# Performance work log

Hardware: AMD Instinct MI355X
Metric: run time of the kernel (lower is better)

## Reference

```python
import jax, jax.numpy as jnp
import numpy as np

B, S, D, H, F = 2, 2048, 1024, 16, 4096
DH = D // H
EPS = 1e-6


def layer_norm(x, g, b):
    mu = jnp.mean(x, axis=-1, keepdims=True)
    var = jnp.mean(jnp.square(x - mu), axis=-1, keepdims=True)
    return (x - mu) * jax.lax.rsqrt(var + EPS) * g + b


def setup_inputs() -> dict:
    key = jax.random.key(0)
    ks = jax.random.split(key, 12)
    s_in = 1.0 / np.sqrt(D)
    s_ff = 1.0 / np.sqrt(F)
    return {
        "x_enc": jax.random.normal(ks[0], (B, S, D), jnp.float32),
        "x_pos": jax.random.normal(ks[1], (B, S, D), jnp.float32),
        "wq": jax.random.normal(ks[2], (D, D), jnp.float32) * s_in,
        "bq": jnp.zeros((D,), jnp.float32),
        "wk": jax.random.normal(ks[3], (D, D), jnp.float32) * s_in,
        "bk": jnp.zeros((D,), jnp.float32),
        "wv": jax.random.normal(ks[4], (D, D), jnp.float32) * s_in,
        "bv": jnp.zeros((D,), jnp.float32),
        "wc": jax.random.normal(ks[5], (D, D), jnp.float32) * s_in,
        "bc": jnp.zeros((D,), jnp.float32),
        "w1": jax.random.normal(ks[6], (D, F), jnp.float32) * s_in,
        "b1": jnp.zeros((F,), jnp.float32),
        "w2": jax.random.normal(ks[7], (F, D), jnp.float32) * s_ff,
        "b2": jnp.zeros((D,), jnp.float32),
        "g1": jnp.ones((D,), jnp.float32),
        "be1": jnp.zeros((D,), jnp.float32),
        "g2": jnp.ones((D,), jnp.float32),
        "be2": jnp.zeros((D,), jnp.float32),
    }


def reference(x_enc, x_pos, wq, bq, wk, bk, wv, bv, wc, bc, w1, b1, w2, b2, g1, be1, g2, be2):
    x = x_enc + x_pos  # [B,S,D]

    def split_heads(t):  # [B,S,D] -> [B,H,S,DH]
        return t.reshape(B, S, H, DH).transpose(0, 2, 1, 3)

    q = split_heads(x @ wq + bq)
    k = split_heads(x @ wk + bk)
    v = split_heads(x @ wv + bv)

    scale = jax.lax.rsqrt(jnp.asarray(DH, jnp.float32))
    logits = jnp.einsum("bhqd,bhkd->bhqk", q, k) * scale  # [B,H,S,S]
    weights = jax.nn.softmax(logits, axis=-1)
    attn = jnp.einsum("bhqk,bhkd->bhqd", weights, v)  # [B,H,S,DH]
    attn = attn.transpose(0, 2, 1, 3).reshape(B, S, D)
    attn = attn @ wc + bc

    # residual: x + LN(attn_out)   (dropout inactive in eval)
    a = x + layer_norm(attn, g1, be1)
    ffn = jnp.maximum(a @ w1 + b1, 0.0) @ w2 + b2
    out = a + layer_norm(ffn, g2, be2)
    return out
```

## Files before the change

### kernel.cpp

```cpp
#include <hip/hip_runtime.h>
#include <math.h>

#define B_ 2
#define S_ 2048
#define D_ 1024
#define H_ 16
#define F_ 4096

typedef __bf16 bf16_t;
typedef __bf16 bf16x8 __attribute__((ext_vector_type(8)));
typedef __bf16 bf16x4 __attribute__((ext_vector_type(4)));
typedef float f32x4 __attribute__((ext_vector_type(4)));
typedef float f32x16 __attribute__((ext_vector_type(16)));
typedef _Float16 f16x4 __attribute__((ext_vector_type(4)));
typedef _Float16 f16x8 __attribute__((ext_vector_type(8)));
typedef __fp16 h16x2 __attribute__((ext_vector_type(2)));

__device__ __forceinline__ bf16_t f2b(float f) { return (bf16_t)f; }

__device__ __forceinline__ void gld_lds16(const void* g, void* l) {
  __builtin_amdgcn_global_load_lds(
      (const __attribute__((address_space(1))) unsigned int*)g,
      (__attribute__((address_space(3))) unsigned int*)l, 16, 0, 0);
}

__device__ __forceinline__ void transpose_tile(const float* __restrict__ in,
                                               bf16_t* __restrict__ out,
                                               int K, int N, int bx, int by) {
  __shared__ float tile[64][65];
  int k0 = by * 64, n0 = bx * 64;
  int tid = threadIdx.x;
  int col4 = tid & 15;
  int row = tid >> 4;
#pragma unroll
  for (int rr = 0; rr < 4; ++rr) {
    int r = rr * 16 + row;
    float4 v = *reinterpret_cast<const float4*>(in + (size_t)(k0 + r) * N + n0 + col4 * 4);
    tile[r][col4 * 4 + 0] = v.x;
    tile[r][col4 * 4 + 1] = v.y;
    tile[r][col4 * 4 + 2] = v.z;
    tile[r][col4 * 4 + 3] = v.w;
  }
  __syncthreads();
#pragma unroll
  for (int rr = 0; rr < 4; ++rr) {
    int n = rr * 16 + row;
    bf16x4 o;
    o[0] = f2b(tile[col4 * 4 + 0][n]);
    o[1] = f2b(tile[col4 * 4 + 1][n]);
    o[2] = f2b(tile[col4 * 4 + 2][n]);
    o[3] = f2b(tile[col4 * 4 + 3][n]);
    *reinterpret_cast<bf16x4*>(out + (size_t)(n0 + n) * K + k0 + col4 * 4) = o;
  }
}

__global__ __launch_bounds__(256) void prep_kernel(
    const float* __restrict__ xe, const float* __restrict__ xp,
    bf16_t* __restrict__ XB,
    const float* __restrict__ wq, const float* __restrict__ wk,
    const float* __restrict__ wv, const float* __restrict__ wc,
    const float* __restrict__ w1, const float* __restrict__ w2,
    const float* __restrict__ bq, const float* __restrict__ bk,
    const float* __restrict__ bv,
    bf16_t* __restrict__ Wqkvt, bf16_t* __restrict__ wctb,
    bf16_t* __restrict__ w1tb, bf16_t* __restrict__ w2tb,
    float* __restrict__ bqkv) {
  int bid = blockIdx.x;
  if (bid < 4096) {
    int i = bid * 256 + threadIdx.x;
    float4 av = reinterpret_cast<const float4*>(xe)[i];
    float4 bv4 = reinterpret_cast<const float4*>(xp)[i];
    bf16x4 o;
    o[0] = f2b(av.x + bv4.x); o[1] = f2b(av.y + bv4.y);
    o[2] = f2b(av.z + bv4.z); o[3] = f2b(av.w + bv4.w);
    reinterpret_cast<bf16x4*>(XB)[i] = o;
    return;
  }
  int pb = bid - 4096;
  if (pb < 1024) {
    int seg = pb >> 8, local = pb & 255;
    const float* src = seg == 0 ? wq : (seg == 1 ? wk : (seg == 2 ? wv : wc));
    bf16_t* dst = seg == 3 ? wctb : Wqkvt + (size_t)seg * D_ * D_;
    transpose_tile(src, dst, D_, D_, local & 15, local >> 4);
  } else if (pb < 2048) {
    int local = pb - 1024;
    transpose_tile(w1, w1tb, D_, F_, local & 63, local >> 6);
  } else if (pb < 3072) {
    int local = pb - 2048;
    transpose_tile(w2, w2tb, F_, D_, local & 15, local >> 4);
  } else {
    int i = (pb - 3072) * 256 + threadIdx.x;
    const float* src = i < 1024 ? bq : (i < 2048 ? bk : bv);
    bqkv[i] = src[i & 1023];
  }
}


__device__ __forceinline__ void stage_half(const bf16_t* __restrict__ G,
                                           int grow0, int K, int kt,
                                           bf16_t* lb, int tid) {
#pragma unroll
  for (int c = 0; c < 2; ++c) {
    int e = c * 512 + tid;
    int rl = e >> 3, kg = e & 7;
    int kgs = kg ^ (rl & 7);
    gld_lds16(G + (size_t)(grow0 + rl) * K + kt + kgs * 8, lb + e * 8);
  }
}

template <int DBUF, int MH, int NH, int SARR, int SBUF, int SH, int DOWAIT>
__device__ __forceinline__ void gemm_phase(
    bf16_t* As, bf16_t* Bs, const bf16_t* __restrict__ A,
    const bf16_t* __restrict__ Bt, f32x16 (&acc)[4][2], int bm, int bn, int K,
    int kbeg, int stile, int tid, int m32, int khalf, int ra0, int ra1, int rb) {
  const bf16_t* abase = As + (DBUF * 2 + MH) * 8192;
  const bf16_t* bbase = Bs + (DBUF * 2 + NH) * 8192;
  bf16x8 af0[4], af1[4], bfx[4];
#pragma unroll
  for (int kc = 0; kc < 4; ++kc) {
    int kg = ((kc * 2 + khalf) ^ (m32 & 7)) * 8;
    af0[kc] = *reinterpret_cast<const bf16x8*>(abase + ra0 * 64 + kg);
    af1[kc] = *reinterpret_cast<const bf16x8*>(abase + ra1 * 64 + kg);
    bfx[kc] = *reinterpret_cast<const bf16x8*>(bbase + rb * 64 + kg);
  }
  {
    const bf16_t* G = SARR ? Bt : A;
    int g0 = (SARR ? bn : bm) + SH * 128;
    bf16_t* lb = (SARR ? Bs : As) + (SBUF * 2 + SH) * 8192;
    stage_half(G, g0, K, kbeg + stile * 64, lb, tid);
  }
  if (DOWAIT) asm volatile("s_waitcnt vmcnt(4)" ::: "memory");
  __builtin_amdgcn_s_barrier();
  asm volatile("s_waitcnt lgkmcnt(0)" ::: "memory");
  __builtin_amdgcn_sched_barrier(0);
  __builtin_amdgcn_s_setprio(1);
#pragma unroll
  for (int kc = 0; kc < 4; ++kc) {
    acc[MH * 2 + 0][NH] = __builtin_amdgcn_mfma_f32_32x32x16_bf16(
        af0[kc], bfx[kc], acc[MH * 2 + 0][NH], 0, 0, 0);
    acc[MH * 2 + 1][NH] = __builtin_amdgcn_mfma_f32_32x32x16_bf16(
        af1[kc], bfx[kc], acc[MH * 2 + 1][NH], 0, 0, 0);
  }
  __builtin_amdgcn_s_setprio(0);
  __builtin_amdgcn_s_barrier();
}

__global__ __launch_bounds__(512) void gemm_kernel(
    const bf16_t* __restrict__ A, const bf16_t* __restrict__ Bt,
    const float* __restrict__ bias,
    bf16_t* __restrict__ P0, bf16_t* __restrict__ P1,
    bf16_t* __restrict__ P2, bf16_t* __restrict__ P3,
    _Float16* __restrict__ VTout,
    int M, int N, int K, int relu, int kchunk, int rx, int ry) {
  __shared__ bf16_t As[4 * 8192];
  __shared__ bf16_t Bs[4 * 8192];
  int tid = threadIdx.x;
  int lane = tid & 63, wave = tid >> 6;
  int bx = blockIdx.x, by = blockIdx.y;
  if (rx) {
    int id = by * gridDim.x + bx;
    int j = id & 7, local = id >> 3;
    int regs_x = gridDim.x / rx;
    bx = (j % regs_x) * rx + local % rx;
    by = (j / regs_x) * ry + local / rx;
  }
  int bm = by * 256, bn = bx * 256;
  int wm = wave >> 2, wn = wave & 3;
  int m32 = lane & 31, khalf = lane >> 5;
  int ra0 = wm * 64 + m32, ra1 = ra0 + 32, rb = wn * 32 + m32;
  int z = blockIdx.z;
  int kbeg = z * kchunk;
  int nt = kchunk >> 6, ntm1 = nt - 1;
  f32x16 acc[4][2] = {};

  stage_half(A, bm, K, kbeg, As + 0 * 8192, tid);
  stage_half(Bt, bn, K, kbeg, Bs + 0 * 8192, tid);
  stage_half(A, bm + 128, K, kbeg, As + 1 * 8192, tid);
  stage_half(Bt, bn + 128, K, kbeg, Bs + 1 * 8192, tid);
  stage_half(A, bm, K, kbeg + 64, As + 2 * 8192, tid);
  stage_half(Bt, bn, K, kbeg + 64, Bs + 2 * 8192, tid);
  asm volatile("s_waitcnt vmcnt(4)" ::: "memory");
  __builtin_amdgcn_s_barrier();

  int nt2 = nt >> 1;
  for (int j = 0; j < nt2; ++j) {
    int t1 = 2 * j + 1;
    int t2 = 2 * j + 2 > ntm1 ? ntm1 : 2 * j + 2;
    int t3 = 2 * j + 3 > ntm1 ? ntm1 : 2 * j + 3;
    gemm_phase<0, 0, 0, 0, 1, 1, 0>(As, Bs, A, Bt, acc, bm, bn, K, kbeg, t1, tid, m32, khalf, ra0, ra1, rb);
    gemm_phase<0, 0, 1, 1, 1, 1, 0>(As, Bs, A, Bt, acc, bm, bn, K, kbeg, t1, tid, m32, khalf, ra0, ra1, rb);
    gemm_phase<0, 1, 0, 0, 0, 0, 0>(As, Bs, A, Bt, acc, bm, bn, K, kbeg, t2, tid, m32, khalf, ra0, ra1, rb);
    gemm_phase<0, 1, 1, 1, 0, 0, 1>(As, Bs, A, Bt, acc, bm, bn, K, kbeg, t2, tid, m32, khalf, ra0, ra1, rb);
    gemm_phase<1, 0, 0, 0, 0, 1, 0>(As, Bs, A, Bt, acc, bm, bn, K, kbeg, t2, tid, m32, khalf, ra0, ra1, rb);
    gemm_phase<1, 0, 1, 1, 0, 1, 0>(As, Bs, A, Bt, acc, bm, bn, K, kbeg, t2, tid, m32, khalf, ra0, ra1, rb);
    gemm_phase<1, 1, 0, 0, 1, 0, 0>(As, Bs, A, Bt, acc, bm, bn, K, kbeg, t3, tid, m32, khalf, ra0, ra1, rb);
    gemm_phase<1, 1, 1, 1, 1, 0, 1>(As, Bs, A, Bt, acc, bm, bn, K, kbeg, t3, tid, m32, khalf, ra0, ra1, rb);
  }

  bf16_t* Cb = z == 0 ? P0 : (z == 1 ? P1 : (z == 2 ? P2 : P3));
#pragma unroll
  for (int ni = 0; ni < 2; ++ni) {
    int n = bn + ni * 128 + wn * 32 + m32;
    float bz = (bias && z == 0) ? bias[n] : 0.f;
#pragma unroll
    for (int mi = 0; mi < 4; ++mi) {
      float vv[16];
#pragma unroll
      for (int r = 0; r < 16; ++r) {
        float v = acc[mi][ni][r] + bz;
        if (relu) v = fmaxf(v, 0.f);
        vv[r] = v;
      }
      int sb = bm + (mi >> 1) * 128 + wm * 64 + (mi & 1) * 32;
      if (VTout && n >= 2048) {
        int h = (n - 2048) >> 6, d = (n - 2048) & 63;
        int bb = sb >> 11;
        _Float16* vtr = VTout + ((size_t)((bb * H_ + h) * 64 + d)) * S_ + (sb & 2047);
#pragma unroll
        for (int g = 0; g < 4; ++g) {
          int off = ((2 * g + khalf) & 3) * 8 + (g >> 1) * 4;
          f16x4 hv;
          hv[0] = (_Float16)vv[g * 4 + 0]; hv[1] = (_Float16)vv[g * 4 + 1];
          hv[2] = (_Float16)vv[g * 4 + 2]; hv[3] = (_Float16)vv[g * 4 + 3];
          *reinterpret_cast<f16x4*>(vtr + off) = hv;
        }
      } else {
#pragma unroll
        for (int r = 0; r < 16; ++r) {
          int m = sb + (r & 3) + 8 * (r >> 2) + 4 * khalf;
          Cb[(size_t)m * N + n] = f2b(vv[r]);
        }
      }
    }
  }
}

__global__ __launch_bounds__(512) void attn_kernel(const bf16_t* __restrict__ Q,
                                                   const bf16_t* __restrict__ Kg,
                                                   const _Float16* __restrict__ VT,
                                                   bf16_t* __restrict__ O, int ldq) {
  __shared__ bf16_t Ks[2][128 * 64];
  __shared__ _Float16 Vs[2][64 * 128];
  int qt = blockIdx.x, h = blockIdx.y, b = blockIdx.z;
  int tid = threadIdx.x, wave = tid >> 6, lane = tid & 63;
  int qcol = lane & 15, grp = lane >> 4;
  int qbase = qt * 128 + wave * 16;
  const float kS = 0.125f * 1.4426950408889634f;
  const float kB = 12.0f * 1.4426950408889634f;
  const h16x2 one2 = {(__fp16)1.f, (__fp16)1.f};

  bf16x8 qf[2];
#pragma unroll
  for (int c = 0; c < 2; ++c)
    qf[c] = *reinterpret_cast<const bf16x8*>(
        Q + (size_t)(b * S_ + qbase + qcol) * ldq + h * 64 + c * 32 + grp * 8);
  const _Float16* vtb = VT + (size_t)((b * H_ + h) * 64) * S_;

  f32x4 oacc[4] = {};
  float lsum = 0.f;

#define ATTN_STAGE(BUF, T0)                                                     \
  {                                                                             \
    _Pragma("unroll") for (int cc = 0; cc < 2; ++cc) {                          \
      int e = cc * 512 + tid;                                                   \
      int row = e >> 3, kg = e & 7, kgs = kg ^ (row & 7);                       \
      gld_lds16(Kg + (size_t)(b * S_ + (T0) + row) * ldq + h * 64 + kgs * 8,    \
                &Ks[BUF][0] + e * 8);                                           \
    }                                                                           \
    _Pragma("unroll") for (int cc = 0; cc < 2; ++cc) {                          \
      int e = cc * 512 + tid;                                                   \
      int d = e >> 4, kc = e & 15, kcs = kc ^ (d & 7);                          \
      gld_lds16(vtb + (size_t)d * S_ + (T0) + kcs * 8, &Vs[BUF][0] + e * 8);    \
    }                                                                           \
  }

  ATTN_STAGE(0, 0);
  __syncthreads();

  int buf = 0;
  for (int t0 = 0; t0 < S_; t0 += 128) {
    if (t0 + 128 < S_) {
      if (buf == 0) ATTN_STAGE(1, t0 + 128) else ATTN_STAGE(0, t0 + 128);
    }
    const bf16_t* ksb = &Ks[buf][0];
    const _Float16* vsb = &Vs[buf][0];
#pragma unroll
    for (int kb2 = 0; kb2 < 4; ++kb2) {
      f32x4 se = {}, so = {};
      int krowe = kb2 * 32 + qcol;
      int krowo = krowe + 16;
#pragma unroll
      for (int c = 0; c < 2; ++c) {
        int gce = (c * 4 + grp) ^ (krowe & 7);
        bf16x8 kfe = *reinterpret_cast<const bf16x8*>(ksb + krowe * 64 + gce * 8);
        se = __builtin_amdgcn_mfma_f32_16x16x32_bf16(kfe, qf[c], se, 0, 0, 0);
        int gco = (c * 4 + grp) ^ (krowo & 7);
        bf16x8 kfo = *reinterpret_cast<const bf16x8*>(ksb + krowo * 64 + gco * 8);
        so = __builtin_amdgcn_mfma_f32_16x16x32_bf16(kfo, qf[c], so, 0, 0, 0);
      }
      float pe0 = __builtin_amdgcn_exp2f(fmaf(se[0], kS, -kB));
      float pe1 = __builtin_amdgcn_exp2f(fmaf(se[1], kS, -kB));
      float pe2 = __builtin_amdgcn_exp2f(fmaf(se[2], kS, -kB));
      float pe3 = __builtin_amdgcn_exp2f(fmaf(se[3], kS, -kB));
      float po0 = __builtin_amdgcn_exp2f(fmaf(so[0], kS, -kB));
      float po1 = __builtin_amdgcn_exp2f(fmaf(so[1], kS, -kB));
      float po2 = __builtin_amdgcn_exp2f(fmaf(so[2], kS, -kB));
      float po3 = __builtin_amdgcn_exp2f(fmaf(so[3], kS, -kB));
      h16x2 e01 = __builtin_amdgcn_cvt_pkrtz(pe0, pe1);
      h16x2 e23 = __builtin_amdgcn_cvt_pkrtz(pe2, pe3);
      h16x2 q01 = __builtin_amdgcn_cvt_pkrtz(po0, po1);
      h16x2 q23 = __builtin_amdgcn_cvt_pkrtz(po2, po3);
      lsum = __builtin_amdgcn_fdot2(e01, one2, lsum, false);
      lsum = __builtin_amdgcn_fdot2(e23, one2, lsum, false);
      lsum = __builtin_amdgcn_fdot2(q01, one2, lsum, false);
      lsum = __builtin_amdgcn_fdot2(q23, one2, lsum, false);
      f16x8 pf;
      pf[0] = (_Float16)e01[0]; pf[1] = (_Float16)e01[1];
      pf[2] = (_Float16)e23[0]; pf[3] = (_Float16)e23[1];
      pf[4] = (_Float16)q01[0]; pf[5] = (_Float16)q01[1];
      pf[6] = (_Float16)q23[0]; pf[7] = (_Float16)q23[1];
      __builtin_amdgcn_s_setprio(1);
#pragma unroll
      for (int db = 0; db < 4; ++db) {
        int d = db * 16 + qcol;
        int kc = (kb2 * 4 + grp) ^ (d & 7);
        f16x8 vf = *reinterpret_cast<const f16x8*>(vsb + d * 128 + kc * 8);
        oacc[db] = __builtin_amdgcn_mfma_f32_16x16x32_f16(vf, pf, oacc[db], 0, 0, 0);
      }
      __builtin_amdgcn_s_setprio(0);
    }
    __syncthreads();
    buf ^= 1;
  }
#undef ATTN_STAGE

  lsum += __shfl_xor(lsum, 16, 64);
  lsum += __shfl_xor(lsum, 32, 64);
  float inv = 1.f / lsum;
  size_t rowbase = (size_t)(b * S_ + qbase + qcol) * D_ + h * 64;
#pragma unroll
  for (int db = 0; db < 4; ++db)
#pragma unroll
    for (int r = 0; r < 4; ++r)
      O[rowbase + db * 16 + grp * 4 + r] = f2b(oacc[db][r] * inv);
}

__global__ __launch_bounds__(256) void ln_res_kernel(const bf16_t* Y0,
                                                     const bf16_t* Y1,
                                                     const bf16_t* Y2,
                                                     const bf16_t* Y3,
                                                     int nY,
                                                     const bf16_t* Xres,
                                                     const float* __restrict__ g,
                                                     const float* __restrict__ be,
                                                     float* OutF,
                                                     bf16_t* OutB) {
  int row = blockIdx.x;
  int tid = threadIdx.x, wave = tid >> 6, lane = tid & 63;
  size_t base = (size_t)row * D_;
  bf16x4 y0 = reinterpret_cast<const bf16x4*>(Y0 + base)[tid];
  bf16x4 y1 = reinterpret_cast<const bf16x4*>(Y1 + base)[tid];
  float4 v;
  v.x = (float)y0[0] + (float)y1[0];
  v.y = (float)y0[1] + (float)y1[1];
  v.z = (float)y0[2] + (float)y1[2];
  v.w = (float)y0[3] + (float)y1[3];
  if (nY == 4) {
    bf16x4 y2 = reinterpret_cast<const bf16x4*>(Y2 + base)[tid];
    bf16x4 y3 = reinterpret_cast<const bf16x4*>(Y3 + base)[tid];
    v.x += (float)y2[0] + (float)y3[0];
    v.y += (float)y2[1] + (float)y3[1];
    v.z += (float)y2[2] + (float)y3[2];
    v.w += (float)y2[3] + (float)y3[3];
  }
  float s = v.x + v.y + v.z + v.w;
  float s2 = v.x * v.x + v.y * v.y + v.z * v.z + v.w * v.w;
#pragma unroll
  for (int off = 32; off > 0; off >>= 1) {
    s += __shfl_xor(s, off, 64);
    s2 += __shfl_xor(s2, off, 64);
  }
  __shared__ float red[2][4];
  if (lane == 0) { red[0][wave] = s; red[1][wave] = s2; }
  __syncthreads();
  s = red[0][0] + red[0][1] + red[0][2] + red[0][3];
  s2 = red[1][0] + red[1][1] + red[1][2] + red[1][3];
  float mu = s * (1.f / D_);
  float var = s2 * (1.f / D_) - mu * mu;
  float rstd = rsqrtf(var + 1e-6f);
  bf16x4 xr4 = reinterpret_cast<const bf16x4*>(Xres + base)[tid];
  float4 gv = reinterpret_cast<const float4*>(g)[tid];
  float4 bv = reinterpret_cast<const float4*>(be)[tid];
  float4 o;
  o.x = (float)xr4[0] + (v.x - mu) * rstd * gv.x + bv.x;
  o.y = (float)xr4[1] + (v.y - mu) * rstd * gv.y + bv.y;
  o.z = (float)xr4[2] + (v.z - mu) * rstd * gv.z + bv.z;
  o.w = (float)xr4[3] + (v.w - mu) * rstd * gv.w + bv.w;
  if (OutF) reinterpret_cast<float4*>(OutF + base)[tid] = o;
  if (OutB) {
    bf16x4 ob; ob[0] = f2b(o.x); ob[1] = f2b(o.y); ob[2] = f2b(o.z); ob[3] = f2b(o.w);
    reinterpret_cast<bf16x4*>(OutB + base)[tid] = ob;
  }
}

extern "C" void kernel_launch(void* const* d_in, const int* in_sizes, int n_in,
                              void* d_out, int out_size, void* d_ws, size_t ws_size,
                              hipStream_t stream) {
  const float* x_enc = (const float*)d_in[0];
  const float* x_pos = (const float*)d_in[1];
  const float* wq = (const float*)d_in[2];
  const float* bq = (const float*)d_in[3];
  const float* wk = (const float*)d_in[4];
  const float* bk = (const float*)d_in[5];
  const float* wv = (const float*)d_in[6];
  const float* bv = (const float*)d_in[7];
  const float* wc = (const float*)d_in[8];
  const float* bc = (const float*)d_in[9];
  const float* w1 = (const float*)d_in[10];
  const float* b1 = (const float*)d_in[11];
  const float* w2 = (const float*)d_in[12];
  const float* b2 = (const float*)d_in[13];
  const float* g1 = (const float*)d_in[14];
  const float* be1 = (const float*)d_in[15];
  const float* g2 = (const float*)d_in[16];
  const float* be2 = (const float*)d_in[17];

  const size_t MB = 1024ull * 1024ull;
  char* w = (char*)d_ws;
  bf16_t* F0 = (bf16_t*)(w + 0);
  bf16_t* F1p = (bf16_t*)(w + 8 * MB);
  bf16_t* Wqkvt = (bf16_t*)(w + 32 * MB);
  bf16_t* wctb = (bf16_t*)(w + 38 * MB);
  bf16_t* w1tb = (bf16_t*)(w + 40 * MB);
  bf16_t* w2tb = (bf16_t*)(w + 48 * MB);
  bf16_t* XB = (bf16_t*)(w + 56 * MB);
  bf16_t* QKVB = (bf16_t*)(w + 64 * MB);
  bf16_t* Pp0 = (bf16_t*)(w + 64 * MB);
  bf16_t* Pp1 = (bf16_t*)(w + 72 * MB);
  bf16_t* Pp2 = (bf16_t*)(w + 80 * MB);
  bf16_t* F2 = (bf16_t*)(w + 64 * MB);
  bf16_t* F3 = (bf16_t*)(w + 72 * MB);
  bf16_t* ATTNB = (bf16_t*)(w + 88 * MB);
  float* bqkv = (float*)(w + 96 * MB);
  _Float16* VTg = (_Float16*)(w + 104 * MB);
  bf16_t* Pp3 = (bf16_t*)(w + 104 * MB);
  bf16_t* F1B = (bf16_t*)(w + 112 * MB);

  const int rows = B_ * S_;

  prep_kernel<<<7180, 256, 0, stream>>>(x_enc, x_pos, XB,
                                        wq, wk, wv, wc, w1, w2, bq, bk, bv,
                                        Wqkvt, wctb, w1tb, w2tb, bqkv);

  gemm_kernel<<<dim3(3 * D_ / 256, rows / 256, 1), 512, 0, stream>>>(
      XB, Wqkvt, bqkv, QKVB, nullptr, nullptr, nullptr, VTg,
      rows, 3 * D_, D_, 0, D_, 3, 8);

  attn_kernel<<<dim3(S_ / 128, H_, B_), 512, 0, stream>>>(
      QKVB, QKVB + D_, VTg, ATTNB, 3 * D_);

  gemm_kernel<<<dim3(D_ / 256, rows / 256, 4), 512, 0, stream>>>(
      ATTNB, wctb, bc, Pp0, Pp1, Pp2, Pp3, nullptr,
      rows, D_, D_, 0, D_ / 4, 2, 4);

  ln_res_kernel<<<rows, 256, 0, stream>>>(Pp0, Pp1, Pp2, Pp3, 4, XB, g1, be1,
                                          nullptr, XB);

  gemm_kernel<<<dim3(F_ / 256, rows / 256, 1), 512, 0, stream>>>(
      XB, w1tb, b1, F1B, nullptr, nullptr, nullptr, nullptr,
      rows, F_, D_, 1, D_, 4, 8);

  gemm_kernel<<<dim3(D_ / 256, rows / 256, 4), 512, 0, stream>>>(
      F1B, w2tb, b2, F0, F1p, F2, F3, nullptr,
      rows, D_, F_, 0, F_ / 4, 2, 4);

  ln_res_kernel<<<rows, 256, 0, stream>>>(F0, F1p, F2, F3, 4, XB, g2, be2,
                                          (float*)d_out, nullptr);
}
```

Measured before the change: 376.3 us.

## Merge GEMM main loop into four phases with register-cached B fragments

```diff
diff --git a/kernel.cpp b/kernel.cpp
--- a/kernel.cpp
+++ b/kernel.cpp
@@ -108,27 +108,26 @@
   }
 }
 
-template <int DBUF, int MH, int NH, int SARR, int SBUF, int SH, int DOWAIT>
-__device__ __forceinline__ void gemm_phase(
+template <int DBUF, int MH, int SSLOT, int DOWAIT>
+__device__ __forceinline__ void gemm_phase4(
     bf16_t* As, bf16_t* Bs, const bf16_t* __restrict__ A,
-    const bf16_t* __restrict__ Bt, f32x16 (&acc)[4][2], int bm, int bn, int K,
-    int kbeg, int stile, int tid, int m32, int khalf, int ra0, int ra1, int rb) {
+    const bf16_t* __restrict__ Bt, f32x16 (&acc)[4][2], bf16x8 (&bq)[2][4],
+    int bm, int bn, int K, int kt, int tid, int m32, int khalf,
+    int ra0, int ra1, int rb) {
   const bf16_t* abase = As + (DBUF * 2 + MH) * 8192;
-  const bf16_t* bbase = Bs + (DBUF * 2 + NH) * 8192;
-  bf16x8 af0[4], af1[4], bfx[4];
+  bf16x8 af0[4], af1[4];
 #pragma unroll
   for (int kc = 0; kc < 4; ++kc) {
     int kg = ((kc * 2 + khalf) ^ (m32 & 7)) * 8;
     af0[kc] = *reinterpret_cast<const bf16x8*>(abase + ra0 * 64 + kg);
     af1[kc] = *reinterpret_cast<const bf16x8*>(abase + ra1 * 64 + kg);
-    bfx[kc] = *reinterpret_cast<const bf16x8*>(bbase + rb * 64 + kg);
-  }
-  {
-    const bf16_t* G = SARR ? Bt : A;
-    int g0 = (SARR ? bn : bm) + SH * 128;
-    bf16_t* lb = (SARR ? Bs : As) + (SBUF * 2 + SH) * 8192;
-    stage_half(G, g0, K, kbeg + stile * 64, lb, tid);
-  }
+    if (MH == 0) {
+      bq[0][kc] = *reinterpret_cast<const bf16x8*>(Bs + (DBUF * 2 + 0) * 8192 + rb * 64 + kg);
+      bq[1][kc] = *reinterpret_cast<const bf16x8*>(Bs + (DBUF * 2 + 1) * 8192 + rb * 64 + kg);
+    }
+  }
+  stage_half(A, bm + (SSLOT & 1) * 128, K, kt, As + SSLOT * 8192, tid);
+  stage_half(Bt, bn + (SSLOT & 1) * 128, K, kt, Bs + SSLOT * 8192, tid);
   if (DOWAIT) asm volatile("s_waitcnt vmcnt(4)" ::: "memory");
   __builtin_amdgcn_s_barrier();
   asm volatile("s_waitcnt lgkmcnt(0)" ::: "memory");
@@ -136,10 +135,14 @@
   __builtin_amdgcn_s_setprio(1);
 #pragma unroll
   for (int kc = 0; kc < 4; ++kc) {
-    acc[MH * 2 + 0][NH] = __builtin_amdgcn_mfma_f32_32x32x16_bf16(
-        af0[kc], bfx[kc], acc[MH * 2 + 0][NH], 0, 0, 0);
-    acc[MH * 2 + 1][NH] = __builtin_amdgcn_mfma_f32_32x32x16_bf16(
-        af1[kc], bfx[kc], acc[MH * 2 + 1][NH], 0, 0, 0);
+    acc[MH * 2 + 0][0] = __builtin_amdgcn_mfma_f32_32x32x16_bf16(
+        af0[kc], bq[0][kc], acc[MH * 2 + 0][0], 0, 0, 0);
+    acc[MH * 2 + 1][0] = __builtin_amdgcn_mfma_f32_32x32x16_bf16(
+        af1[kc], bq[0][kc], acc[MH * 2 + 1][0], 0, 0, 0);
+    acc[MH * 2 + 0][1] = __builtin_amdgcn_mfma_f32_32x32x16_bf16(
+        af0[kc], bq[1][kc], acc[MH * 2 + 0][1], 0, 0, 0);
+    acc[MH * 2 + 1][1] = __builtin_amdgcn_mfma_f32_32x32x16_bf16(
+        af1[kc], bq[1][kc], acc[MH * 2 + 1][1], 0, 0, 0);
   }
   __builtin_amdgcn_s_setprio(0);
   __builtin_amdgcn_s_barrier();
@@ -187,14 +190,11 @@
     int t1 = 2 * j + 1;
     int t2 = 2 * j + 2 > ntm1 ? ntm1 : 2 * j + 2;
     int t3 = 2 * j + 3 > ntm1 ? ntm1 : 2 * j + 3;
-    gemm_phase<0, 0, 0, 0, 1, 1, 0>(As, Bs, A, Bt, acc, bm, bn, K, kbeg, t1, tid, m32, khalf, ra0, ra1, rb);
-    gemm_phase<0, 0, 1, 1, 1, 1, 0>(As, Bs, A, Bt, acc, bm, bn, K, kbeg, t1, tid, m32, khalf, ra0, ra1, rb);
-    gemm_phase<0, 1, 0, 0, 0, 0, 0>(As, Bs, A, Bt, acc, bm, bn, K, kbeg, t2, tid, m32, khalf, ra0, ra1, rb);
-    gemm_phase<0, 1, 1, 1, 0, 0, 1>(As, Bs, A, Bt, acc, bm, bn, K, kbeg, t2, tid, m32, khalf, ra0, ra1, rb);
-    gemm_phase<1, 0, 0, 0, 0, 1, 0>(As, Bs, A, Bt, acc, bm, bn, K, kbeg, t2, tid, m32, khalf, ra0, ra1, rb);
-    gemm_phase<1, 0, 1, 1, 0, 1, 0>(As, Bs, A, Bt, acc, bm, bn, K, kbeg, t2, tid, m32, khalf, ra0, ra1, rb);
-    gemm_phase<1, 1, 0, 0, 1, 0, 0>(As, Bs, A, Bt, acc, bm, bn, K, kbeg, t3, tid, m32, khalf, ra0, ra1, rb);
-    gemm_phase<1, 1, 1, 1, 1, 0, 1>(As, Bs, A, Bt, acc, bm, bn, K, kbeg, t3, tid, m32, khalf, ra0, ra1, rb);
+    bf16x8 bq[2][4];
+    gemm_phase4<0, 0, 3, 0>(As, Bs, A, Bt, acc, bq, bm, bn, K, kbeg + t1 * 64, tid, m32, khalf, ra0, ra1, rb);
+    gemm_phase4<0, 1, 0, 1>(As, Bs, A, Bt, acc, bq, bm, bn, K, kbeg + t2 * 64, tid, m32, khalf, ra0, ra1, rb);
+    gemm_phase4<1, 0, 1, 0>(As, Bs, A, Bt, acc, bq, bm, bn, K, kbeg + t2 * 64, tid, m32, khalf, ra0, ra1, rb);
+    gemm_phase4<1, 1, 2, 1>(As, Bs, A, Bt, acc, bq, bm, bn, K, kbeg + t3 * 64, tid, m32, khalf, ra0, ra1, rb);
   }
 
   bf16_t* Cb = z == 0 ? P0 : (z == 1 ? P1 : (z == 2 ? P2 : P3));
```

Result: faster. 355.1 us (-5.6%).
